# Kernel optimization log

Hardware: AMD Instinct MI355X
Metric: run time of the kernel (lower is better)

## Reference

```python
import jax, jax.numpy as jnp
import numpy as np


def _dwconv3(x, w, b):
    # Depthwise conv1d, kernel=3, 'same' padding, channels_first.
    # x: [B, Cs, L], w: [3, Cs], b: [Cs]
    xp = jnp.pad(x, ((0, 0), (0, 0), (1, 1)))
    return (w[0][:, None] * xp[:, :, :-2]
            + w[1][:, None] * xp[:, :, 1:-1]
            + w[2][:, None] * xp[:, :, 2:]
            + b[:, None])


def setup_inputs() -> dict:
    key = jax.random.key(0)
    ks = jax.random.split(key, 3)
    B, C, L, S = 32, 256, 4096, 8
    return {
        "inputs": jax.random.normal(ks[0], (B, C, L), jnp.float32),
        "conv_w": jax.random.normal(ks[1], (S, 3, C // S), jnp.float32) * 0.3,
        "conv_b": jnp.zeros((S, C // S), jnp.float32),
        "ln_gamma": jnp.ones((L,), jnp.float32),
        "ln_beta": jnp.zeros((L,), jnp.float32),
        "pw_w": jax.random.normal(ks[2], (C,), jnp.float32) * 0.3,
        "pw_b": jnp.zeros((C,), jnp.float32),
    }


def reference(inputs, conv_w, conv_b, ln_gamma, ln_beta, pw_w, pw_b):
    S = conv_w.shape[0]
    xs = jnp.split(inputs, S, axis=1)  # each [B, C/S, L]
    # sequential recurrence: y_i = dwconv_i(x_i + y_{i-1})
    y = _dwconv3(xs[0], conv_w[0], conv_b[0])
    ys = [y]
    for i in range(1, S):
        y = _dwconv3(xs[i] + y, conv_w[i], conv_b[i])
        ys.append(y)
    y = jnp.concatenate(ys, axis=1)  # [B, C, L]
    # keras LayerNormalization(axis=-1): normalize over time axis L
    mean = jnp.mean(y, axis=-1, keepdims=True)
    var = jnp.var(y, axis=-1, keepdims=True)
    y = (y - mean) * jax.lax.rsqrt(var + 1e-6) * ln_gamma + ln_beta
    # depthwise k=1 conv (per-channel scale + bias) then exact gelu
    y = jax.nn.gelu(y * pw_w[None, :, None] + pw_b[None, :, None], approximate=False)
    return inputs + y
```

## Files before the change

kernel.cpp:

```cpp
#include <hip/hip_runtime.h>
#include <math.h>

#define BB   32
#define CC   256
#define LL   4096
#define SS   8
#define CS   32
#define NT   256
#define F4_ROW (LL / 4)
#define F4_THR (F4_ROW / NT)

__device__ __forceinline__ float gelu_exact(float x) {
    return 0.5f * x * (1.0f + erff(x * 0.70710678118654752440f));
}

__global__ __launch_bounds__(NT, 4)
void hdconv_encoder_kernel(const float* __restrict__ inp,
                           const float* __restrict__ conv_w,
                           const float* __restrict__ conv_b,
                           const float* __restrict__ ln_g,
                           const float* __restrict__ ln_b,
                           const float* __restrict__ pw_w,
                           const float* __restrict__ pw_b,
                           float* __restrict__ out) {
    __shared__ float4 S4[F4_ROW];
    __shared__ float  red[8];
    __shared__ float  bcast[2];

    const int t    = threadIdx.x;
    const int blk  = blockIdx.x;
    const int b    = blk >> 5;
    const int c    = blk & 31;
    const int lane = t & 63;
    const int wave = t >> 6;

    float y[16];
#pragma unroll
    for (int j = 0; j < 16; ++j) y[j] = 0.0f;

    float4 g4[F4_THR], e4[F4_THR];
    const float4* gp = (const float4*)ln_g;
    const float4* ep = (const float4*)ln_b;
#pragma unroll
    for (int k = 0; k < F4_THR; ++k) {
        g4[k] = gp[t + NT * k];
        e4[k] = ep[t + NT * k];
    }

    for (int i = 0; i < SS; ++i) {
        const int ch = i * CS + c;
        const float4* xrow = (const float4*)(inp + ((size_t)(b * CC + ch)) * LL);
        float4*       orow = (float4*)(out + ((size_t)(b * CC + ch)) * LL);

        float4 x4[F4_THR];
#pragma unroll
        for (int k = 0; k < F4_THR; ++k) x4[k] = xrow[t + NT * k];
#pragma unroll
        for (int k = 0; k < F4_THR; ++k) {
            float4 s;
            s.x = x4[k].x + y[4 * k + 0];
            s.y = x4[k].y + y[4 * k + 1];
            s.z = x4[k].z + y[4 * k + 2];
            s.w = x4[k].w + y[4 * k + 3];
            S4[t + NT * k] = s;
        }
        __syncthreads();

        const float w0 = conv_w[i * 96 + 0 * CS + c];
        const float w1 = conv_w[i * 96 + 1 * CS + c];
        const float w2 = conv_w[i * 96 + 2 * CS + c];
        const float bb = conv_b[i * CS + c];

        float lsum = 0.0f, lsq = 0.0f;
#pragma unroll
        for (int k = 0; k < F4_THR; ++k) {
            const int f = t + NT * k;
            const float4 cc = S4[f];
            const float sm1 = (f > 0)          ? S4[f - 1].w : 0.0f;
            const float sp4 = (f < F4_ROW - 1) ? S4[f + 1].x : 0.0f;
            float y0 = fmaf(w0, sm1,  fmaf(w1, cc.x, fmaf(w2, cc.y, bb)));
            float y1 = fmaf(w0, cc.x, fmaf(w1, cc.y, fmaf(w2, cc.z, bb)));
            float y2 = fmaf(w0, cc.y, fmaf(w1, cc.z, fmaf(w2, cc.w, bb)));
            float y3 = fmaf(w0, cc.z, fmaf(w1, cc.w, fmaf(w2, sp4, bb)));
            y[4 * k + 0] = y0; y[4 * k + 1] = y1;
            y[4 * k + 2] = y2; y[4 * k + 3] = y3;
            lsum += (y0 + y1) + (y2 + y3);
            lsq  += fmaf(y0, y0, fmaf(y1, y1, fmaf(y2, y2, y3 * y3)));
        }

#pragma unroll
        for (int off = 32; off > 0; off >>= 1) {
            lsum += __shfl_down(lsum, off, 64);
            lsq  += __shfl_down(lsq,  off, 64);
        }
        if (lane == 0) { red[wave * 2] = lsum; red[wave * 2 + 1] = lsq; }
        __syncthreads();
        if (t == 0) {
            const float sum = (red[0] + red[2]) + (red[4] + red[6]);
            const float sq  = (red[1] + red[3]) + (red[5] + red[7]);
            const float mean = sum * (1.0f / LL);
            const float var  = sq * (1.0f / LL) - mean * mean;
            bcast[0] = mean;
            bcast[1] = rsqrtf(var + 1e-6f);
        }
        __syncthreads();
        const float mean = bcast[0];
        const float inv  = bcast[1];

        const float pw = pw_w[ch];
        const float pb = pw_b[ch];
#pragma unroll
        for (int k = 0; k < F4_THR; ++k) {
            float4 o;
            float n;
            n   = fmaf((y[4 * k + 0] - mean) * inv, g4[k].x, e4[k].x);
            o.x = x4[k].x + gelu_exact(fmaf(n, pw, pb));
            n   = fmaf((y[4 * k + 1] - mean) * inv, g4[k].y, e4[k].y);
            o.y = x4[k].y + gelu_exact(fmaf(n, pw, pb));
            n   = fmaf((y[4 * k + 2] - mean) * inv, g4[k].z, e4[k].z);
            o.z = x4[k].z + gelu_exact(fmaf(n, pw, pb));
            n   = fmaf((y[4 * k + 3] - mean) * inv, g4[k].w, e4[k].w);
            o.w = x4[k].w + gelu_exact(fmaf(n, pw, pb));
            orow[t + NT * k] = o;
        }
    }
}

extern "C" void kernel_launch(void* const* d_in, const int* in_sizes, int n_in,
                              void* d_out, int out_size, void* d_ws, size_t ws_size,
                              hipStream_t stream) {
    const float* inp    = (const float*)d_in[0];
    const float* conv_w = (const float*)d_in[1];
    const float* conv_b = (const float*)d_in[2];
    const float* ln_g   = (const float*)d_in[3];
    const float* ln_b   = (const float*)d_in[4];
    const float* pw_w   = (const float*)d_in[5];
    const float* pw_b   = (const float*)d_in[6];
    float* out = (float*)d_out;

    dim3 grid(BB * CS);
    dim3 block(NT);
    hdconv_encoder_kernel<<<grid, block, 0, stream>>>(
        inp, conv_w, conv_b, ln_g, ln_b, pw_w, pw_b, out);
}
```

Baseline: 250.3 us.

## Prefetch next split row, use wave shuffles for conv halo, cut barriers

Replaces the full-row LDS staging with in-register wave shuffles for the 3-tap neighbors. Only wave-boundary halo values go through small double-buffered LDS arrays. The next channel row's input is prefetched into registers during the current iteration to overlap global loads with compute. Barriers per iteration drop from three to one, each thread computes mean/var itself, and output stores become nontemporal. This raises register pressure (an extra 16 floats for the prefetch), which may lower occupancy.

Measured after the change: 265.3 us. 6.0% more time.

```diff
diff --git a/kernel.cpp b/kernel.cpp
--- a/kernel.cpp
+++ b/kernel.cpp
@@ -10,8 +10,16 @@
 #define F4_ROW (LL / 4)
 #define F4_THR (F4_ROW / NT)
 
+typedef float f4 __attribute__((ext_vector_type(4)));
+
 __device__ __forceinline__ float gelu_exact(float x) {
     return 0.5f * x * (1.0f + erff(x * 0.70710678118654752440f));
+}
+
+__device__ __forceinline__ void lds_barrier() {
+    asm volatile("s_waitcnt lgkmcnt(0)" ::: "memory");
+    __builtin_amdgcn_s_barrier();
+    asm volatile("" ::: "memory");
 }
 
 __global__ __launch_bounds__(NT, 4)
@@ -23,9 +31,9 @@
                            const float* __restrict__ pw_w,
                            const float* __restrict__ pw_b,
                            float* __restrict__ out) {
-    __shared__ float4 S4[F4_ROW];
-    __shared__ float  red[8];
-    __shared__ float  bcast[2];
+    __shared__ float eW[2][17];
+    __shared__ float eX[2][17];
+    __shared__ float red[2][8];
 
     const int t    = threadIdx.x;
     const int blk  = blockIdx.x;
@@ -34,37 +42,51 @@
     const int lane = t & 63;
     const int wave = t >> 6;
 
+    if (t == 0) {
+        eW[0][0]  = 0.0f; eW[1][0]  = 0.0f;
+        eX[0][16] = 0.0f; eX[1][16] = 0.0f;
+    }
+
     float y[16];
 #pragma unroll
     for (int j = 0; j < 16; ++j) y[j] = 0.0f;
 
     float4 g4[F4_THR], e4[F4_THR];
-    const float4* gp = (const float4*)ln_g;
-    const float4* ep = (const float4*)ln_b;
+    {
+        const float4* gp = (const float4*)ln_g;
+        const float4* ep = (const float4*)ln_b;
+#pragma unroll
+        for (int k = 0; k < F4_THR; ++k) {
+            g4[k] = gp[t + NT * k];
+            e4[k] = ep[t + NT * k];
+        }
+    }
+
+    f4 x4[F4_THR];
+    {
+        const f4* xrow = (const f4*)(inp + ((size_t)(b * CC + c)) * LL);
+#pragma unroll
+        for (int k = 0; k < F4_THR; ++k) x4[k] = xrow[t + NT * k];
+    }
+
 #pragma unroll
     for (int k = 0; k < F4_THR; ++k) {
-        g4[k] = gp[t + NT * k];
-        e4[k] = ep[t + NT * k];
+        const int kw = k * 4 + wave;
+        if (lane == 63) eW[0][1 + kw] = x4[k].w;
+        if (lane == 0)  eX[0][kw]     = x4[k].x;
     }
+    lds_barrier();
 
     for (int i = 0; i < SS; ++i) {
+        const int p  = i & 1;
         const int ch = i * CS + c;
-        const float4* xrow = (const float4*)(inp + ((size_t)(b * CC + ch)) * LL);
-        float4*       orow = (float4*)(out + ((size_t)(b * CC + ch)) * LL);
 
-        float4 x4[F4_THR];
+        f4 xn4[F4_THR];
+        if (i + 1 < SS) {
+            const f4* xn = (const f4*)(inp + ((size_t)(b * CC + ch + CS)) * LL);
 #pragma unroll
-        for (int k = 0; k < F4_THR; ++k) x4[k] = xrow[t + NT * k];
-#pragma unroll
-        for (int k = 0; k < F4_THR; ++k) {
-            float4 s;
-            s.x = x4[k].x + y[4 * k + 0];
-            s.y = x4[k].y + y[4 * k + 1];
-            s.z = x4[k].z + y[4 * k + 2];
-            s.w = x4[k].w + y[4 * k + 3];
-            S4[t + NT * k] = s;
+            for (int k = 0; k < F4_THR; ++k) xn4[k] = xn[t + NT * k];
         }
-        __syncthreads();
 
         const float w0 = conv_w[i * 96 + 0 * CS + c];
         const float w1 = conv_w[i * 96 + 1 * CS + c];
@@ -74,14 +96,19 @@
         float lsum = 0.0f, lsq = 0.0f;
 #pragma unroll
         for (int k = 0; k < F4_THR; ++k) {
-            const int f = t + NT * k;
-            const float4 cc = S4[f];
-            const float sm1 = (f > 0)          ? S4[f - 1].w : 0.0f;
-            const float sp4 = (f < F4_ROW - 1) ? S4[f + 1].x : 0.0f;
-            float y0 = fmaf(w0, sm1,  fmaf(w1, cc.x, fmaf(w2, cc.y, bb)));
-            float y1 = fmaf(w0, cc.x, fmaf(w1, cc.y, fmaf(w2, cc.z, bb)));
-            float y2 = fmaf(w0, cc.y, fmaf(w1, cc.z, fmaf(w2, cc.w, bb)));
-            float y3 = fmaf(w0, cc.z, fmaf(w1, cc.w, fmaf(w2, sp4, bb)));
+            const int kw = k * 4 + wave;
+            const float s0 = x4[k].x + y[4 * k + 0];
+            const float s1 = x4[k].y + y[4 * k + 1];
+            const float s2 = x4[k].z + y[4 * k + 2];
+            const float s3 = x4[k].w + y[4 * k + 3];
+            float sm1 = __shfl_up(s3, 1, 64);
+            float sp4 = __shfl_down(s0, 1, 64);
+            if (lane == 0)  sm1 = eW[p][kw];
+            if (lane == 63) sp4 = eX[p][kw + 1];
+            const float y0 = fmaf(w0, sm1, fmaf(w1, s0, fmaf(w2, s1, bb)));
+            const float y1 = fmaf(w0, s0,  fmaf(w1, s1, fmaf(w2, s2, bb)));
+            const float y2 = fmaf(w0, s1,  fmaf(w1, s2, fmaf(w2, s3, bb)));
+            const float y3 = fmaf(w0, s2,  fmaf(w1, s3, fmaf(w2, sp4, bb)));
             y[4 * k + 0] = y0; y[4 * k + 1] = y1;
             y[4 * k + 2] = y2; y[4 * k + 3] = y3;
             lsum += (y0 + y1) + (y2 + y3);
@@ -93,25 +120,31 @@
             lsum += __shfl_down(lsum, off, 64);
             lsq  += __shfl_down(lsq,  off, 64);
         }
-        if (lane == 0) { red[wave * 2] = lsum; red[wave * 2 + 1] = lsq; }
-        __syncthreads();
-        if (t == 0) {
-            const float sum = (red[0] + red[2]) + (red[4] + red[6]);
-            const float sq  = (red[1] + red[3]) + (red[5] + red[7]);
-            const float mean = sum * (1.0f / LL);
-            const float var  = sq * (1.0f / LL) - mean * mean;
-            bcast[0] = mean;
-            bcast[1] = rsqrtf(var + 1e-6f);
+        if (lane == 0) { red[p][wave * 2] = lsum; red[p][wave * 2 + 1] = lsq; }
+
+        if (i + 1 < SS) {
+#pragma unroll
+            for (int k = 0; k < F4_THR; ++k) {
+                const int kw = k * 4 + wave;
+                if (lane == 63) eW[p ^ 1][1 + kw] = xn4[k].w + y[4 * k + 3];
+                if (lane == 0)  eX[p ^ 1][kw]     = xn4[k].x + y[4 * k + 0];
+            }
         }
-        __syncthreads();
-        const float mean = bcast[0];
-        const float inv  = bcast[1];
+
+        lds_barrier();
+
+        const float sum = (red[p][0] + red[p][2]) + (red[p][4] + red[p][6]);
+        const float sq  = (red[p][1] + red[p][3]) + (red[p][5] + red[p][7]);
+        const float mean = sum * (1.0f / LL);
+        const float var  = sq * (1.0f / LL) - mean * mean;
+        const float inv  = rsqrtf(var + 1e-6f);
 
         const float pw = pw_w[ch];
         const float pb = pw_b[ch];
+        f4* orow = (f4*)(out + ((size_t)(b * CC + ch)) * LL);
 #pragma unroll
         for (int k = 0; k < F4_THR; ++k) {
-            float4 o;
+            f4 o;
             float n;
             n   = fmaf((y[4 * k + 0] - mean) * inv, g4[k].x, e4[k].x);
             o.x = x4[k].x + gelu_exact(fmaf(n, pw, pb));
@@ -121,7 +154,12 @@
             o.z = x4[k].z + gelu_exact(fmaf(n, pw, pb));
             n   = fmaf((y[4 * k + 3] - mean) * inv, g4[k].w, e4[k].w);
             o.w = x4[k].w + gelu_exact(fmaf(n, pw, pb));
-            orow[t + NT * k] = o;
+            __builtin_nontemporal_store(o, &orow[t + NT * k]);
+        }
+
+        if (i + 1 < SS) {
+#pragma unroll
+            for (int k = 0; k < F4_THR; ++k) x4[k] = xn4[k];
         }
     }
 }
```
